# Kernel optimization log

Measured on AMD Instinct MI355X. Metric: run time of the kernel, lower is better.

## Reference

```python
import jax, jax.numpy as jnp
import numpy as np

NUM_CODE = 1024
DIM_CODE = 256
EPS = 1e-6


def setup_inputs() -> dict:
    key = jax.random.key(0)
    kz, ke = jax.random.split(key)
    z = jax.random.normal(kz, (32, 256, 32, 32), dtype=jnp.float32)
    # torch init: uniform(-1/num_code, 1/num_code)
    emb = jax.random.uniform(ke, (NUM_CODE, DIM_CODE), dtype=jnp.float32,
                             minval=-1.0 / NUM_CODE, maxval=1.0 / NUM_CODE)
    return {"z": z, "emb": emb}


def _l2norm(x, axis=-1):
    # F.normalize(p=2): x / max(||x||, eps_torch); torch default eps=1e-12
    n = jnp.sqrt(jnp.sum(x * x, axis=axis, keepdims=True))
    return x / jnp.maximum(n, 1e-12)


def reference(z, emb):
    N, C, H, W = z.shape
    z_flat = jnp.transpose(z, (0, 2, 3, 1)).reshape(N * H * W, C)  # (T, C)
    zn = _l2norm(z_flat, axis=1)
    en = _l2norm(emb, axis=1)
    # squared euclidean distance between normalized vectors
    d = (jnp.sum(zn * zn, axis=1, keepdims=True)
         + jnp.sum(en * en, axis=1)
         - 2.0 * jnp.matmul(zn, en.T))            # (T, K)
    min_idx = jnp.argmin(d, axis=1)               # (T,)
    quant = jnp.take(emb, min_idx, axis=0)        # (T, C) — gather of RAW codebook
    quant = jnp.transpose(quant.reshape(N, H, W, C), (0, 3, 1, 2))  # NCHW
    index = min_idx.reshape(N, H, W)
    return quant, index
```

## Files before the change

### kernel.cpp

```cpp
#include <hip/hip_runtime.h>

#define NTOK 32768
#define CDIM 256
#define KCODE 1024
#define C4 64

typedef __bf16 bf16x8 __attribute__((ext_vector_type(8)));
typedef float  f32x4  __attribute__((ext_vector_type(4)));
typedef const __attribute__((address_space(1))) void* as1cvp;
typedef __attribute__((address_space(3))) void* as3vp;

__device__ __forceinline__ unsigned long long umin64(unsigned long long a, unsigned long long b) { return a < b ? a : b; }
__device__ __forceinline__ unsigned long long umax64(unsigned long long a, unsigned long long b) { return a > b ? a : b; }

__global__ void k_norm_emb(const float* __restrict__ emb,
                           float* __restrict__ en, float* __restrict__ en2,
                           __bf16* __restrict__ eh, __bf16* __restrict__ el) {
    int k = blockIdx.x;
    int l = threadIdx.x;
    float4 v = reinterpret_cast<const float4*>(emb)[k * C4 + l];
    float ss = v.x*v.x + v.y*v.y + v.z*v.z + v.w*v.w;
    #pragma unroll
    for (int o = 32; o >= 1; o >>= 1) ss += __shfl_xor(ss, o, 64);
    float den = fmaxf(sqrtf(ss), 1e-12f);
    float4 e;
    e.x = v.x / den; e.y = v.y / den; e.z = v.z / den; e.w = v.w / den;
    reinterpret_cast<float4*>(en)[k * C4 + l] = e;
    float s2 = e.x*e.x + e.y*e.y + e.z*e.z + e.w*e.w;
    #pragma unroll
    for (int o = 32; o >= 1; o >>= 1) s2 += __shfl_xor(s2, o, 64);
    if (l == 0) en2[k] = s2;

    __bf16* ehp = eh + (size_t)k * CDIM + 4 * l;
    __bf16* elp = el + (size_t)k * CDIM + 4 * l;
    float ev[4] = {e.x, e.y, e.z, e.w};
    #pragma unroll
    for (int q = 0; q < 4; ++q) {
        __bf16 h = (__bf16)ev[q];
        ehp[q] = h;
        elp[q] = (__bf16)(ev[q] - (float)h);
    }
}

__global__ void k_norm_z(const float* __restrict__ z,
                         float* __restrict__ znt, float* __restrict__ znt2) {
    __shared__ float zsb[CDIM * 32];
    __shared__ float ssp[256];
    __shared__ float dens[32];
    int tid = threadIdx.x;
    int t0  = blockIdx.x * 32;
    int n   = t0 >> 10;
    int thw0 = t0 & 1023;

    int l = tid & 31, grp = tid >> 5;
    const float* zb = z + (((size_t)(n * CDIM)) << 10) + thw0 + l;
    float ss = 0.f;
    int c0 = grp * 32;
    for (int cc = 0; cc < 32; ++cc) {
        int c = c0 + cc;
        float v = zb[((size_t)c) << 10];
        zsb[c * 32 + ((l + c) & 31)] = v;
        ss += v * v;
    }
    ssp[tid] = ss;
    __syncthreads();
    if (tid < 32) {
        float tot = 0.f;
        #pragma unroll
        for (int g = 0; g < 8; ++g) tot += ssp[g * 32 + tid];
        dens[tid] = fmaxf(sqrtf(tot), 1e-12f);
    }
    __syncthreads();

    int l2 = tid & 63, tg = tid >> 6;
    for (int it = 0; it < 8; ++it) {
        int tok = tg * 8 + it;
        float den = dens[tok];
        float s2 = 0.f;
        #pragma unroll
        for (int cq = 0; cq < 4; ++cq) {
            int c = cq * 64 + l2;
            float v = zsb[c * 32 + ((tok + c) & 31)] / den;
            znt[((size_t)(t0 + tok)) * CDIM + c] = v;
            s2 += v * v;
        }
        #pragma unroll
        for (int o = 32; o >= 1; o >>= 1) s2 += __shfl_xor(s2, o, 64);
        if (l2 == 0) znt2[t0 + tok] = s2;
    }
}

__global__ __launch_bounds__(256, 2) void k_mfma(
        const float* __restrict__ znt,
        const __bf16* __restrict__ eh, const __bf16* __restrict__ el,
        const float* __restrict__ en2g,
        const float* __restrict__ znt2, const float* __restrict__ en,
        const float* __restrict__ emb, float* __restrict__ out) {
    __shared__ __align__(16) char smem_u[69632];
    __shared__ unsigned long long t2l[64][2][2];
    __shared__ int idxs[64];
    __bf16* ebuf = reinterpret_cast<__bf16*>(smem_u);
    float*  en2s = reinterpret_cast<float*>(smem_u + 65536);
    float*  qt   = reinterpret_cast<float*>(smem_u);

    int tid = threadIdx.x;
    int l = tid & 63, wid = tid >> 6;
    int mw = wid >> 1, nw = wid & 1;
    int t0 = blockIdx.x * 64;
    int row = l & 15, kg = l >> 4;

    for (int i = tid; i < KCODE; i += 256) en2s[i] = en2g[i];

    bf16x8 ah[2][8], al_[2][8];
    #pragma unroll
    for (int mt = 0; mt < 2; ++mt) {
        size_t tok = (size_t)(t0 + mw * 32 + mt * 16 + row);
        const float* pz = znt + tok * CDIM + kg * 8;
        #pragma unroll
        for (int ks = 0; ks < 8; ++ks) {
            float f[8];
            *reinterpret_cast<float4*>(&f[0]) = *reinterpret_cast<const float4*>(pz + ks * 32);
            *reinterpret_cast<float4*>(&f[4]) = *reinterpret_cast<const float4*>(pz + ks * 32 + 4);
            bf16x8 h, lo;
            #pragma unroll
            for (int q = 0; q < 8; ++q) {
                __bf16 hv = (__bf16)f[q];
                h[q] = hv;
                lo[q] = (__bf16)(f[q] - (float)hv);
            }
            ah[mt][ks] = h; al_[mt][ks] = lo;
        }
    }

    unsigned long long b1[8], b2[8];
    #pragma unroll
    for (int i = 0; i < 8; ++i) { b1[i] = ~0ull; b2[i] = ~0ull; }

    auto stage = [&](int buf, int ch) {
        #pragma unroll
        for (int a = 0; a < 2; ++a) {
            const __bf16* src = a ? el : eh;
            #pragma unroll
            for (int i2 = 0; i2 < 4; ++i2) {
                int s = i2 * 256 + tid;
                int code = s >> 5, c16 = s & 31;
                int gslot = c16 ^ (code & 15);
                const __bf16* gp = src + ((size_t)(ch * 32 + code)) * CDIM + gslot * 8;
                __bf16* ld = ebuf + (size_t)(buf * 2 + a) * 8192 + (size_t)(i2 * 256 + wid * 64) * 8;
                __builtin_amdgcn_global_load_lds((as1cvp)gp, (as3vp)ld, 16, 0, 0);
            }
        }
    };

    stage(0, 0);
    __syncthreads();
    #pragma unroll 2
    for (int ch = 0; ch < 32; ++ch) {
        int cur = ch & 1;
        if (ch < 31) stage(cur ^ 1, ch + 1);

        const __bf16* bh_base = ebuf + (size_t)(cur * 2 + 0) * 8192;
        const __bf16* bl_base = ebuf + (size_t)(cur * 2 + 1) * 8192;

        f32x4 a0[2], a1[2], a2[2];
        #pragma unroll
        for (int mt = 0; mt < 2; ++mt)
            #pragma unroll
            for (int r = 0; r < 4; ++r) { a0[mt][r] = 0.f; a1[mt][r] = 0.f; a2[mt][r] = 0.f; }

        int code_l = nw * 16 + row;
        #pragma unroll
        for (int ks = 0; ks < 8; ++ks) {
            int slot = (ks * 4 + kg) ^ row;
            bf16x8 bh = *reinterpret_cast<const bf16x8*>(bh_base + code_l * 256 + slot * 8);
            bf16x8 bl = *reinterpret_cast<const bf16x8*>(bl_base + code_l * 256 + slot * 8);
            #pragma unroll
            for (int mt = 0; mt < 2; ++mt) {
                a0[mt] = __builtin_amdgcn_mfma_f32_16x16x32_bf16(ah[mt][ks],  bh, a0[mt], 0, 0, 0);
                a1[mt] = __builtin_amdgcn_mfma_f32_16x16x32_bf16(ah[mt][ks],  bl, a1[mt], 0, 0, 0);
                a2[mt] = __builtin_amdgcn_mfma_f32_16x16x32_bf16(al_[mt][ks], bh, a2[mt], 0, 0, 0);
            }
        }

        int code = ch * 32 + code_l;
        float e2v = en2s[code];
        #pragma unroll
        for (int mt = 0; mt < 2; ++mt)
            #pragma unroll
            for (int r = 0; r < 4; ++r) {
                float d = fmaf(-2.0f, (a0[mt][r] + a1[mt][r]) + a2[mt][r], e2v);
                unsigned ub = __float_as_uint(d);
                ub = (ub & 0x80000000u) ? ~ub : (ub | 0x80000000u);
                unsigned long long key = ((unsigned long long)ub << 32) | (unsigned)code;
                int idx = mt * 4 + r;
                if (key < b1[idx]) { b2[idx] = b1[idx]; b1[idx] = key; }
                else if (key < b2[idx]) { b2[idx] = key; }
            }
        __syncthreads();
    }

    #pragma unroll
    for (int i = 0; i < 8; ++i) {
        #pragma unroll
        for (int off = 1; off < 16; off <<= 1) {
            unsigned long long o1 = __shfl_xor(b1[i], off, 16);
            unsigned long long o2 = __shfl_xor(b2[i], off, 16);
            unsigned long long m1 = umin64(b1[i], o1);
            unsigned long long m2 = umin64(umax64(b1[i], o1), umin64(b2[i], o2));
            b1[i] = m1; b2[i] = m2;
        }
    }
    if ((l & 15) == 0) {
        #pragma unroll
        for (int mt = 0; mt < 2; ++mt)
            #pragma unroll
            for (int r = 0; r < 4; ++r) {
                int tl = mw * 32 + mt * 16 + kg * 4 + r;
                t2l[tl][nw][0] = b1[mt * 4 + r];
                t2l[tl][nw][1] = b2[mt * 4 + r];
            }
    }
    __syncthreads();

    {
        int tl = tid >> 2, q = tid & 3;
        int t = t0 + tl;
        unsigned long long x1 = t2l[tl][0][0], x2 = t2l[tl][0][1];
        unsigned long long y1 = t2l[tl][1][0], y2 = t2l[tl][1][1];
        unsigned c1 = (unsigned)umin64(x1, y1);
        unsigned c2 = (unsigned)umin64(umax64(x1, y1), umin64(x2, y2));
        const float4* zp  = reinterpret_cast<const float4*>(znt) + (size_t)t  * C4 + q * 16;
        const float4* eap = reinterpret_cast<const float4*>(en)  + (size_t)c1 * C4 + q * 16;
        const float4* ebp = reinterpret_cast<const float4*>(en)  + (size_t)c2 * C4 + q * 16;
        float da = 0.f, db = 0.f;
        #pragma unroll
        for (int i = 0; i < 16; ++i) {
            float4 zv = zp[i], av = eap[i], bv = ebp[i];
            da += zv.x*av.x + zv.y*av.y + zv.z*av.z + zv.w*av.w;
            db += zv.x*bv.x + zv.y*bv.y + zv.z*bv.z + zv.w*bv.w;
        }
        da += __shfl_xor(da, 1, 4); da += __shfl_xor(da, 2, 4);
        db += __shfl_xor(db, 1, 4); db += __shfl_xor(db, 2, 4);
        if (q == 0) {
            float z2 = znt2[t];
            float d1 = (z2 + en2s[c1]) - 2.0f * da;
            float d2 = (z2 + en2s[c2]) - 2.0f * db;
            int k = (d2 < d1 || (d2 == d1 && c2 < c1)) ? (int)c2 : (int)c1;
            idxs[tl] = k;
            out[(size_t)NTOK * CDIM + t] = (float)k;
        }
    }
    __syncthreads();

    {
        int tl = tid >> 2, q = tid & 3;
        int kidx = idxs[tl];
        const float4* ep = reinterpret_cast<const float4*>(emb + (size_t)kidx * CDIM + q * 64);
        #pragma unroll
        for (int i = 0; i < 16; ++i) {
            float4 v = ep[i];
            int cb = q * 64 + i * 4;
            qt[tl * 257 + cb + 0] = v.x;
            qt[tl * 257 + cb + 1] = v.y;
            qt[tl * 257 + cb + 2] = v.z;
            qt[tl * 257 + cb + 3] = v.w;
        }
    }
    __syncthreads();

    {
        int hwo = tid & 63, cg = tid >> 6;
        int n = t0 >> 10, hw = (t0 & 1023) + hwo;
        float* ob = out + (size_t)n * (CDIM * 1024) + hw;
        #pragma unroll 8
        for (int cc = 0; cc < 64; ++cc) {
            int c = cg * 64 + cc;
            ob[(size_t)c * 1024] = qt[hwo * 257 + c];
        }
    }
}

extern "C" void kernel_launch(void* const* d_in, const int* in_sizes, int n_in,
                              void* d_out, int out_size, void* d_ws, size_t ws_size,
                              hipStream_t stream) {
    const float* z   = (const float*)d_in[0];
    const float* emb = (const float*)d_in[1];
    float* out  = (float*)d_out;

    float*  en   = (float*)d_ws;
    float*  en2  = en + (size_t)KCODE * CDIM;
    float*  znt2 = en2 + KCODE;
    __bf16* eh   = (__bf16*)(znt2 + NTOK);
    __bf16* el   = eh + (size_t)KCODE * CDIM;
    float*  znt  = (float*)(el + (size_t)KCODE * CDIM);

    k_norm_emb<<<KCODE, 64, 0, stream>>>(emb, en, en2, eh, el);
    k_norm_z<<<NTOK / 32, 256, 0, stream>>>(z, znt, znt2);
    k_mfma<<<NTOK / 64, 256, 0, stream>>>(znt, eh, el, en2, znt2, en, emb, out);
}
```

Before: 100.9 us.

## Merge codebook and token normalization kernels; use float top-2 tracking

Folds the codebook normalization into the token-normalization kernel as 16 extra blocks, which removes one kernel launch. The top-2 candidate tracking replaces its packed 64-bit keys with separate float value and int index registers, so each comparison is a float compare instead of a 64-bit one. The shuffle merge now does tie-breaking on the index explicitly. The gather that writes the quantized vectors remaps its thread-to-token assignment. The float version costs more shuffles and registers in the reduction, and codebook blocks now use strided per-thread stores.

```diff
diff --git a/kernel.cpp b/kernel.cpp
--- a/kernel.cpp
+++ b/kernel.cpp
@@ -10,44 +10,49 @@
 typedef const __attribute__((address_space(1))) void* as1cvp;
 typedef __attribute__((address_space(3))) void* as3vp;
 
-__device__ __forceinline__ unsigned long long umin64(unsigned long long a, unsigned long long b) { return a < b ? a : b; }
-__device__ __forceinline__ unsigned long long umax64(unsigned long long a, unsigned long long b) { return a > b ? a : b; }
-
-__global__ void k_norm_emb(const float* __restrict__ emb,
-                           float* __restrict__ en, float* __restrict__ en2,
-                           __bf16* __restrict__ eh, __bf16* __restrict__ el) {
-    int k = blockIdx.x;
-    int l = threadIdx.x;
-    float4 v = reinterpret_cast<const float4*>(emb)[k * C4 + l];
-    float ss = v.x*v.x + v.y*v.y + v.z*v.z + v.w*v.w;
-    #pragma unroll
-    for (int o = 32; o >= 1; o >>= 1) ss += __shfl_xor(ss, o, 64);
-    float den = fmaxf(sqrtf(ss), 1e-12f);
-    float4 e;
-    e.x = v.x / den; e.y = v.y / den; e.z = v.z / den; e.w = v.w / den;
-    reinterpret_cast<float4*>(en)[k * C4 + l] = e;
-    float s2 = e.x*e.x + e.y*e.y + e.z*e.z + e.w*e.w;
-    #pragma unroll
-    for (int o = 32; o >= 1; o >>= 1) s2 += __shfl_xor(s2, o, 64);
-    if (l == 0) en2[k] = s2;
-
-    __bf16* ehp = eh + (size_t)k * CDIM + 4 * l;
-    __bf16* elp = el + (size_t)k * CDIM + 4 * l;
-    float ev[4] = {e.x, e.y, e.z, e.w};
-    #pragma unroll
-    for (int q = 0; q < 4; ++q) {
-        __bf16 h = (__bf16)ev[q];
-        ehp[q] = h;
-        elp[q] = (__bf16)(ev[q] - (float)h);
-    }
-}
-
-__global__ void k_norm_z(const float* __restrict__ z,
-                         float* __restrict__ znt, float* __restrict__ znt2) {
+__global__ void k_prep(const float* __restrict__ z, const float* __restrict__ emb,
+                       float* __restrict__ znt, float* __restrict__ znt2,
+                       float* __restrict__ en, float* __restrict__ en2,
+                       __bf16* __restrict__ eh, __bf16* __restrict__ el) {
     __shared__ float zsb[CDIM * 32];
     __shared__ float ssp[256];
     __shared__ float dens[32];
     int tid = threadIdx.x;
+
+    if (blockIdx.x >= 1024) {
+        int k = (blockIdx.x - 1024) * 64 + (tid >> 2);
+        int q = tid & 3;
+        const float4* ep = reinterpret_cast<const float4*>(emb) + (size_t)k * C4 + q * 16;
+        float4 v[16];
+        float ss = 0.f;
+        #pragma unroll
+        for (int i = 0; i < 16; ++i) {
+            v[i] = ep[i];
+            ss += v[i].x*v[i].x + v[i].y*v[i].y + v[i].z*v[i].z + v[i].w*v[i].w;
+        }
+        ss += __shfl_xor(ss, 1, 4); ss += __shfl_xor(ss, 2, 4);
+        float den = fmaxf(sqrtf(ss), 1e-12f);
+        float s2 = 0.f;
+        float4* enp = reinterpret_cast<float4*>(en) + (size_t)k * C4 + q * 16;
+        __bf16* ehp = eh + (size_t)k * CDIM + q * 64;
+        __bf16* elp = el + (size_t)k * CDIM + q * 64;
+        #pragma unroll
+        for (int i = 0; i < 16; ++i) {
+            float e4[4] = {v[i].x / den, v[i].y / den, v[i].z / den, v[i].w / den};
+            enp[i] = make_float4(e4[0], e4[1], e4[2], e4[3]);
+            #pragma unroll
+            for (int j = 0; j < 4; ++j) {
+                s2 += e4[j] * e4[j];
+                __bf16 h = (__bf16)e4[j];
+                ehp[i * 4 + j] = h;
+                elp[i * 4 + j] = (__bf16)(e4[j] - (float)h);
+            }
+        }
+        s2 += __shfl_xor(s2, 1, 4); s2 += __shfl_xor(s2, 2, 4);
+        if (q == 0) en2[k] = s2;
+        return;
+    }
+
     int t0  = blockIdx.x * 32;
     int n   = t0 >> 10;
     int thw0 = t0 & 1023;
@@ -97,7 +102,7 @@
         const float* __restrict__ znt2, const float* __restrict__ en,
         const float* __restrict__ emb, float* __restrict__ out) {
     __shared__ __align__(16) char smem_u[69632];
-    __shared__ unsigned long long t2l[64][2][2];
+    __shared__ uint4 t2l[64][2];
     __shared__ int idxs[64];
     __bf16* ebuf = reinterpret_cast<__bf16*>(smem_u);
     float*  en2s = reinterpret_cast<float*>(smem_u + 65536);
@@ -132,9 +137,9 @@
         }
     }
 
-    unsigned long long b1[8], b2[8];
+    float v1f[8], v2f[8]; int i1a[8], i2a[8];
     #pragma unroll
-    for (int i = 0; i < 8; ++i) { b1[i] = ~0ull; b2[i] = ~0ull; }
+    for (int i = 0; i < 8; ++i) { v1f[i] = 3.4e38f; v2f[i] = 3.4e38f; i1a[i] = 0; i2a[i] = 0; }
 
     auto stage = [&](int buf, int ch) {
         #pragma unroll
@@ -189,12 +194,14 @@
             #pragma unroll
             for (int r = 0; r < 4; ++r) {
                 float d = fmaf(-2.0f, (a0[mt][r] + a1[mt][r]) + a2[mt][r], e2v);
-                unsigned ub = __float_as_uint(d);
-                ub = (ub & 0x80000000u) ? ~ub : (ub | 0x80000000u);
-                unsigned long long key = ((unsigned long long)ub << 32) | (unsigned)code;
                 int idx = mt * 4 + r;
-                if (key < b1[idx]) { b2[idx] = b1[idx]; b1[idx] = key; }
-                else if (key < b2[idx]) { b2[idx] = key; }
+                bool lt2 = d < v2f[idx];
+                bool lt1 = d < v1f[idx];
+                if (lt2) {
+                    v2f[idx] = lt1 ? v1f[idx] : d;
+                    i2a[idx] = lt1 ? i1a[idx] : code;
+                    if (lt1) { v1f[idx] = d; i1a[idx] = code; }
+                }
             }
         __syncthreads();
     }
@@ -203,11 +210,14 @@
     for (int i = 0; i < 8; ++i) {
         #pragma unroll
         for (int off = 1; off < 16; off <<= 1) {
-            unsigned long long o1 = __shfl_xor(b1[i], off, 16);
-            unsigned long long o2 = __shfl_xor(b2[i], off, 16);
-            unsigned long long m1 = umin64(b1[i], o1);
-            unsigned long long m2 = umin64(umax64(b1[i], o1), umin64(b2[i], o2));
-            b1[i] = m1; b2[i] = m2;
+            float ov1 = __shfl_xor(v1f[i], off, 16); int oi1 = __shfl_xor(i1a[i], off, 16);
+            float ov2 = __shfl_xor(v2f[i], off, 16); int oi2 = __shfl_xor(i2a[i], off, 16);
+            bool w = (ov1 < v1f[i]) || (ov1 == v1f[i] && oi1 < i1a[i]);
+            float lv = w ? v1f[i] : ov1; int li = w ? i1a[i] : oi1;
+            float s2v = w ? ov2 : v2f[i]; int s2i = w ? oi2 : i2a[i];
+            v1f[i] = w ? ov1 : v1f[i]; i1a[i] = w ? oi1 : i1a[i];
+            bool s = (lv < s2v) || (lv == s2v && li < s2i);
+            v2f[i] = s ? lv : s2v; i2a[i] = s ? li : s2i;
         }
     }
     if ((l & 15) == 0) {
@@ -216,8 +226,9 @@
             #pragma unroll
             for (int r = 0; r < 4; ++r) {
                 int tl = mw * 32 + mt * 16 + kg * 4 + r;
-                t2l[tl][nw][0] = b1[mt * 4 + r];
-                t2l[tl][nw][1] = b2[mt * 4 + r];
+                int i = mt * 4 + r;
+                t2l[tl][nw] = make_uint4(__float_as_uint(v1f[i]), (unsigned)i1a[i],
+                                         __float_as_uint(v2f[i]), (unsigned)i2a[i]);
             }
     }
     __syncthreads();
@@ -225,10 +236,18 @@
     {
         int tl = tid >> 2, q = tid & 3;
         int t = t0 + tl;
-        unsigned long long x1 = t2l[tl][0][0], x2 = t2l[tl][0][1];
-        unsigned long long y1 = t2l[tl][1][0], y2 = t2l[tl][1][1];
-        unsigned c1 = (unsigned)umin64(x1, y1);
-        unsigned c2 = (unsigned)umin64(umax64(x1, y1), umin64(x2, y2));
+        uint4 A = t2l[tl][0], B = t2l[tl][1];
+        float av1 = __uint_as_float(A.x); int ai1 = (int)A.y;
+        float av2 = __uint_as_float(A.z); int ai2 = (int)A.w;
+        float bv1 = __uint_as_float(B.x); int bi1 = (int)B.y;
+        float bv2 = __uint_as_float(B.z); int bi2 = (int)B.w;
+        bool w = (bv1 < av1) || (bv1 == av1 && bi1 < ai1);
+        int   c1 = w ? bi1 : ai1;
+        float lv = w ? av1 : bv1; int li = w ? ai1 : bi1;
+        float wv2 = w ? bv2 : av2; int wi2 = w ? bi2 : ai2;
+        bool s = (lv < wv2) || (lv == wv2 && li < wi2);
+        int   c2 = s ? li : wi2;
+
         const float4* zp  = reinterpret_cast<const float4*>(znt) + (size_t)t  * C4 + q * 16;
         const float4* eap = reinterpret_cast<const float4*>(en)  + (size_t)c1 * C4 + q * 16;
         const float4* ebp = reinterpret_cast<const float4*>(en)  + (size_t)c2 * C4 + q * 16;
@@ -245,7 +264,7 @@
             float z2 = znt2[t];
             float d1 = (z2 + en2s[c1]) - 2.0f * da;
             float d2 = (z2 + en2s[c2]) - 2.0f * db;
-            int k = (d2 < d1 || (d2 == d1 && c2 < c1)) ? (int)c2 : (int)c1;
+            int k = (d2 < d1 || (d2 == d1 && c2 < c1)) ? c2 : c1;
             idxs[tl] = k;
             out[(size_t)NTOK * CDIM + t] = (float)k;
         }
@@ -253,7 +272,7 @@
     __syncthreads();
 
     {
-        int tl = tid >> 2, q = tid & 3;
+        int tl = tid & 63, q = tid >> 6;
         int kidx = idxs[tl];
         const float4* ep = reinterpret_cast<const float4*>(emb + (size_t)kidx * CDIM + q * 64);
         #pragma unroll
@@ -294,7 +313,6 @@
     __bf16* el   = eh + (size_t)KCODE * CDIM;
     float*  znt  = (float*)(el + (size_t)KCODE * CDIM);
 
-    k_norm_emb<<<KCODE, 64, 0, stream>>>(emb, en, en2, eh, el);
-    k_norm_z<<<NTOK / 32, 256, 0, stream>>>(z, znt, znt2);
+    k_prep<<<1024 + 16, 256, 0, stream>>>(z, emb, znt, znt2, en, en2, eh, el);
     k_mfma<<<NTOK / 64, 256, 0, stream>>>(znt, eh, el, en2, znt2, en, emb, out);
 }
```

New measurement: 117.0 us. 16.0% more time.
